# Optimization experiments

Measured on AMD Instinct MI355X. Metric: run time of the kernel, lower is better.

Reference implementation:

```python
import math
import jax, jax.numpy as jnp
import numpy as np

H = 4            # num_attention_heads
EPS = 1e-5       # InstanceNorm / LayerNorm eps (torch default)


def _inorm(x):
    # nn.InstanceNorm1d applied to (N, S, d): normalizes over the last dim per (item, token), no affine
    m = jnp.mean(x, axis=-1, keepdims=True)
    v = jnp.var(x, axis=-1, keepdims=True)
    return (x - m) / jnp.sqrt(v + EPS)


def _tree_layer(x, Wqkv, bqkv, Wo, bo, W1, b1, W2, b2):
    # x: (N, S, d) with S=2
    N, S, d = x.shape
    dh = d // H
    qkv = x @ Wqkv.T + bqkv                      # (N, S, 3d)
    q, k, v = jnp.split(qkv, 3, axis=-1)
    q = q.reshape(N, S, H, dh)
    k = k.reshape(N, S, H, dh)
    v = v.reshape(N, S, H, dh)
    scores = jnp.einsum('nqhd,nkhd->nhqk', q, k) / math.sqrt(dh)
    att = jax.nn.softmax(scores, axis=-1)
    o = jnp.einsum('nhqk,nkhd->nqhd', att, v).reshape(N, S, d)
    o = o @ Wo.T + bo
    x = _inorm(x + o)
    f = jax.nn.gelu(x @ W1.T + b1, approximate=False) @ W2.T + b2
    return _inorm(x + f)


def _mlp(x, Wa, ba, Wb, bb):
    return jax.nn.gelu(x @ Wa.T + ba, approximate=False) @ Wb.T + bb


def setup_inputs() -> dict:
    key = jax.random.key(0)
    ks = jax.random.split(key, 16)
    B, G, d, ff, L, c = 64, 1024, 256, 1024, 4, 128
    s = 0.02
    r = lambda i, shape: (jax.random.normal(ks[i], shape, jnp.float32) * s)
    return dict(
        children=jax.random.normal(ks[0], (B, G, 2, d), jnp.float32),
        roles=r(1, (3, d)),
        Wqkv=r(2, (L, 3 * d, d)), bqkv=jnp.zeros((L, 3 * d), jnp.float32),
        Wo=r(3, (L, d, d)), bo=jnp.zeros((L, d), jnp.float32),
        W1=r(4, (L, ff, d)), b1=jnp.zeros((L, ff), jnp.float32),
        W2=r(5, (L, d, ff)), b2=jnp.zeros((L, d), jnp.float32),
        Wl1=r(6, (d, d)), bl1=jnp.zeros(d, jnp.float32),
        Wl2=r(7, (c, d)), bl2=jnp.zeros(c, jnp.float32),
        Wr1=r(8, (d, d)), br1=jnp.zeros(d, jnp.float32),
        Wr2=r(9, (c, d)), br2=jnp.zeros(c, jnp.float32),
        ln_g=jnp.ones(d, jnp.float32), ln_b=jnp.zeros(d, jnp.float32),
    )


def reference(children, roles, Wqkv, bqkv, Wo, bo, W1, b1, W2, b2,
              Wl1, bl1, Wl2, bl2, Wr1, br1, Wr2, br2, ln_g, ln_b):
    B, G, _, d = children.shape
    c = Wl2.shape[0]
    L = Wqkv.shape[0]
    # flatten (batch, group) and add inside role embeddings (rows 0,1)
    x = children.reshape(B * G, 2, d) + roles[:2][None, :, :]
    for i in range(L):
        x = _tree_layer(x, Wqkv[i], bqkv[i], Wo[i], bo[i], W1[i], b1[i], W2[i], b2[i])
    out = x.reshape(B, G, 2, d)
    left_const = _mlp(out[:, :, 0, :], Wl1, bl1, Wl2, bl2)   # (B, G, c)
    right_const = _mlp(out[:, :, 1, :], Wr1, br1, Wr2, br2)  # (B, G, c)
    mat_scores = jnp.sum(left_const * right_const, axis=-1) / math.sqrt(c)
    # LayerNorm over last dim of summed children
    s = out.sum(axis=2)
    m = jnp.mean(s, axis=-1, keepdims=True)
    v = jnp.var(s, axis=-1, keepdims=True)
    src = (s - m) / jnp.sqrt(v + EPS) * ln_g + ln_b
    return mat_scores, src
```

## Files before the change

kernel.cpp:

```cpp
#include <hip/hip_runtime.h>
#include <math.h>

#define NLAYER 4
#define DMODEL 256
#define ITEMS  32
#define MROWS  64
#define XS     264
#define BS     520
#define EPSV   1e-5f
#define NWAVES 16

typedef __attribute__((ext_vector_type(8))) short short8;
typedef __attribute__((ext_vector_type(4))) float f32x4;

#define OFF_WQKV 0
#define OFF_WO   786432
#define OFF_W1   1048576
#define OFF_W2   2097152
#define OFF_WL1  3145728
#define OFF_WL2  3211264
#define OFF_WR1  3244032
#define OFF_WR2  3309568
#define WS_ELEMS 3342336

static __device__ __forceinline__ float b2f(short s) {
  return __uint_as_float(((unsigned)(unsigned short)s) << 16);
}
static __device__ __forceinline__ short f2bf(float f) {
  unsigned u = __float_as_uint(f);
  return (short)((u + 0x7fffu + ((u >> 16) & 1u)) >> 16);
}
static __device__ __forceinline__ float gelu_f(float x) {
  return 0.5f * x * (1.0f + erff(x * 0.70710678118654752f));
}

template<int MT, int PAIR>
static __device__ void gemm_lds(const short* A, int as, int rmul, int radd,
                                const short* __restrict__ W,
                                const float* __restrict__ bias,
                                short* Out, int oc0, int oro,
                                int N, int act, int tid)
{
  const int wave = tid >> 6;
  const int lane = tid & 63;
  const int lm = lane & 15;
  const int q  = lane >> 4;
  const int ntiles = N >> 4;
  const f32x4 z = {0.f, 0.f, 0.f, 0.f};
  for (int nb = wave * PAIR; nb < ntiles; nb += NWAVES * PAIR) {
    f32x4 acc[MT][PAIR];
    #pragma unroll
    for (int mt = 0; mt < MT; ++mt)
      #pragma unroll
      for (int p = 0; p < PAIR; ++p) acc[mt][p] = z;
    #pragma unroll 4
    for (int kt = 0; kt < 256; kt += 32) {
      short8 b[PAIR];
      #pragma unroll
      for (int p = 0; p < PAIR; ++p)
        b[p] = *(const short8*)(W + ((nb + p) * 16 + lm) * 256 + kt + q * 8);
      #pragma unroll
      for (int mt = 0; mt < MT; ++mt) {
        short8 a = *(const short8*)(A + (rmul * (mt * 16 + lm) + radd) * as + kt + q * 8);
        #pragma unroll
        for (int p = 0; p < PAIR; ++p)
          acc[mt][p] = __builtin_amdgcn_mfma_f32_16x16x32_bf16(a, b[p], acc[mt][p], 0, 0, 0);
      }
    }
    #pragma unroll
    for (int mt = 0; mt < MT; ++mt) {
      #pragma unroll
      for (int p = 0; p < PAIR; ++p) {
        int col = (nb + p) * 16 + lm;
        float bv = bias[col];
        #pragma unroll
        for (int r = 0; r < 4; ++r) {
          float v = acc[mt][p][r] + bv;
          if (act) v = gelu_f(v);
          Out[(oro + mt * 16 + q * 4 + r) * BS + oc0 + col] = f2bf(v);
        }
      }
    }
  }
}

static __device__ void gemm_acc512(f32x4 acc[4], const short* A,
                                   const short* __restrict__ W, int wc0, int tid)
{
  const int wave = tid >> 6, lane = tid & 63;
  const int lm = lane & 15, q = lane >> 4;
  #pragma unroll 2
  for (int kt = 0; kt < 512; kt += 32) {
    short8 b = *(const short8*)(W + (wave * 16 + lm) * 1024 + wc0 + kt + q * 8);
    #pragma unroll
    for (int mt = 0; mt < 4; ++mt) {
      short8 a = *(const short8*)(A + (mt * 16 + lm) * BS + kt + q * 8);
      acc[mt] = __builtin_amdgcn_mfma_f32_16x16x32_bf16(a, b, acc[mt], 0, 0, 0);
    }
  }
}

static __device__ void inorm_pass(short* Xs_, const short* Bf_, bool addx, int tid)
{
  if (tid >= MROWS * 4) return;
  int r = tid >> 2, sub = tid & 3;
  const short* bp = Bf_ + r * BS + sub * 64;
  short* xp = Xs_ + r * XS + sub * 64;
  float sum = 0.f, sq = 0.f;
  for (int e = 0; e < 64; ++e) {
    float v = b2f(bp[e]);
    if (addx) v += b2f(xp[e]);
    sum += v; sq += v * v;
  }
  sum += __shfl_xor(sum, 1); sq += __shfl_xor(sq, 1);
  sum += __shfl_xor(sum, 2); sq += __shfl_xor(sq, 2);
  float mean = sum * (1.f / 256.f);
  float rstd = rsqrtf(sq * (1.f / 256.f) - mean * mean + EPSV);
  for (int e = 0; e < 64; ++e) {
    float v = b2f(bp[e]);
    if (addx) v += b2f(xp[e]);
    xp[e] = f2bf((v - mean) * rstd);
  }
}

struct PrepArgs {
  const float* src[8];
  int n[8];
  int off[8];
};

__global__ void prep_weights(PrepArgs pa, short* __restrict__ dst, int total)
{
  int idx = blockIdx.x * 256 + threadIdx.x;
  if (idx >= total) return;
  int j = 0, off = idx;
  while (j < 7 && off >= pa.n[j]) { off -= pa.n[j]; ++j; }
  dst[pa.off[j] + off] = f2bf(pa.src[j][off]);
}

__global__ __launch_bounds__(1024)
void fused_encoder(const float* __restrict__ children,
                   const float* __restrict__ roles,
                   const short* __restrict__ ws,
                   const float* __restrict__ g_bqkv,
                   const float* __restrict__ g_bo,
                   const float* __restrict__ g_b1,
                   const float* __restrict__ g_b2,
                   const float* __restrict__ g_bl1, const float* __restrict__ g_bl2,
                   const float* __restrict__ g_br1, const float* __restrict__ g_br2,
                   const float* __restrict__ g_lng, const float* __restrict__ g_lnb,
                   float* __restrict__ out)
{
  __shared__ __align__(16) short Xs[MROWS * XS];
  __shared__ __align__(16) short Bf[MROWS * BS];
  __shared__ float Att[ITEMS * 16];

  const int tid = threadIdx.x;
  const int bid = blockIdx.x;

  {
    const float* src = children + (long)bid * MROWS * DMODEL;
    for (int e = tid * 4; e < MROWS * DMODEL; e += 4096) {
      int row = e >> 8, col = e & 255;
      float4 v = *(const float4*)(src + e);
      const float* rl = roles + (row & 1) * DMODEL + col;
      short* xp = Xs + row * XS + col;
      xp[0] = f2bf(v.x + rl[0]);
      xp[1] = f2bf(v.y + rl[1]);
      xp[2] = f2bf(v.z + rl[2]);
      xp[3] = f2bf(v.w + rl[3]);
    }
  }
  __syncthreads();

  for (int l = 0; l < NLAYER; ++l) {
    const short* Wqkv = ws + OFF_WQKV + l * 768 * 256;
    const short* Wo   = ws + OFF_WO   + l * 256 * 256;
    const short* W1   = ws + OFF_W1   + l * 1024 * 256;
    const short* W2   = ws + OFF_W2   + l * 256 * 1024;

    gemm_lds<4, 2>(Xs, XS, 1, 0, Wqkv, g_bqkv + l * 768, Bf, 0, 0, 512, 0, tid);
    __syncthreads();

    if (tid < ITEMS * 8) {
      int i = tid >> 3, h = (tid >> 1) & 3, tk = tid & 1;
      const short* qp = Bf + (2 * i + tk) * BS + h * 64;
      const short* k0 = Bf + (2 * i    ) * BS + 256 + h * 64;
      const short* k1 = Bf + (2 * i + 1) * BS + 256 + h * 64;
      float s0 = 0.f, s1 = 0.f;
      for (int e = 0; e < 64; ++e) {
        float qv = b2f(qp[e]);
        s0 += qv * b2f(k0[e]);
        s1 += qv * b2f(k1[e]);
      }
      s0 *= 0.125f; s1 *= 0.125f;
      float mx = fmaxf(s0, s1);
      float e0 = __expf(s0 - mx), e1 = __expf(s1 - mx);
      float inv = 1.f / (e0 + e1);
      float* ap = Att + ((i * 4 + h) * 2 + tk) * 2;
      ap[0] = e0 * inv; ap[1] = e1 * inv;
    }
    __syncthreads();

    gemm_lds<4, 1>(Xs, XS, 1, 0, Wqkv + 512 * 256, g_bqkv + l * 768 + 512, Bf, 0, 0, 256, 0, tid);
    __syncthreads();

    if (tid < MROWS * 4) {
      int r = tid >> 2, h = tid & 3;
      int i = r >> 1, tk = r & 1;
      const float* ap = Att + ((i * 4 + h) * 2 + tk) * 2;
      float a0 = ap[0], a1 = ap[1];
      const short* v0 = Bf + (2 * i) * BS + h * 64;
      const short* v1 = Bf + (2 * i + 1) * BS + h * 64;
      short* op = Bf + r * BS + 256 + h * 64;
      for (int e = 0; e < 64; ++e)
        op[e] = f2bf(a0 * b2f(v0[e]) + a1 * b2f(v1[e]));
    }
    __syncthreads();

    gemm_lds<4, 1>(Bf + 256, BS, 1, 0, Wo, g_bo + l * 256, Bf, 0, 0, 256, 0, tid);
    __syncthreads();
    inorm_pass(Xs, Bf, true, tid);
    __syncthreads();

    f32x4 facc[4];
    {
      const f32x4 z = {0.f, 0.f, 0.f, 0.f};
      #pragma unroll
      for (int mt = 0; mt < 4; ++mt) facc[mt] = z;
    }
    for (int ch = 0; ch < 2; ++ch) {
      gemm_lds<4, 2>(Xs, XS, 1, 0, W1 + ch * 512 * 256, g_b1 + l * 1024 + ch * 512,
                     Bf, 0, 0, 512, 1, tid);
      __syncthreads();
      gemm_acc512(facc, Bf, W2, ch * 512, tid);
      __syncthreads();
    }
    {
      const int wave = tid >> 6, lane = tid & 63, lm = lane & 15, q = lane >> 4;
      int col = wave * 16 + lm;
      float bv = g_b2[l * 256 + col];
      #pragma unroll
      for (int mt = 0; mt < 4; ++mt) {
        #pragma unroll
        for (int r = 0; r < 4; ++r) {
          int row = mt * 16 + q * 4 + r;
          Bf[row * BS + col] = f2bf(facc[mt][r] + bv + b2f(Xs[row * XS + col]));
        }
      }
    }
    __syncthreads();
    inorm_pass(Xs, Bf, false, tid);
    __syncthreads();
  }

  gemm_lds<2, 1>(Xs, XS, 2, 0, ws + OFF_WL1, g_bl1, Bf, 0, 0, 256, 1, tid);
  gemm_lds<2, 1>(Xs, XS, 2, 1, ws + OFF_WR1, g_br1, Bf, 256, 0, 256, 1, tid);
  __syncthreads();
  gemm_lds<2, 1>(Bf, BS, 1, 0, ws + OFF_WL2, g_bl2, Bf, 0, 32, 128, 0, tid);
  gemm_lds<2, 1>(Bf + 256, BS, 1, 0, ws + OFF_WR2, g_br2, Bf, 128, 32, 128, 0, tid);
  __syncthreads();

  if (tid < ITEMS * 8) {
    int i = tid >> 3, sub = tid & 7;
    const short* lp = Bf + (32 + i) * BS + sub * 16;
    float acc = 0.f;
    for (int j = 0; j < 16; ++j) acc += b2f(lp[j]) * b2f(lp[128 + j]);
    acc += __shfl_xor(acc, 1);
    acc += __shfl_xor(acc, 2);
    acc += __shfl_xor(acc, 4);
    if (sub == 0) out[bid * ITEMS + i] = acc * 0.088388347648318447f;
  }
  if (tid < ITEMS * 8) {
    int i = tid >> 3, sub = tid & 7;
    const short* x0 = Xs + (2 * i) * XS + sub * 32;
    const short* x1 = Xs + (2 * i + 1) * XS + sub * 32;
    float sum = 0.f, sq = 0.f;
    for (int e = 0; e < 32; ++e) {
      float v = b2f(x0[e]) + b2f(x1[e]);
      sum += v; sq += v * v;
    }
    sum += __shfl_xor(sum, 1); sq += __shfl_xor(sq, 1);
    sum += __shfl_xor(sum, 2); sq += __shfl_xor(sq, 2);
    sum += __shfl_xor(sum, 4); sq += __shfl_xor(sq, 4);
    float mean = sum * (1.f / 256.f);
    float rstd = rsqrtf(sq * (1.f / 256.f) - mean * mean + EPSV);
    float* op = out + 65536 + ((long)bid * ITEMS + i) * DMODEL + sub * 32;
    for (int e = 0; e < 32; ++e) {
      int c = sub * 32 + e;
      float v = b2f(x0[e]) + b2f(x1[e]);
      op[e] = (v - mean) * rstd * g_lng[c] + g_lnb[c];
    }
  }
}

extern "C" void kernel_launch(void* const* d_in, const int* in_sizes, int n_in,
                              void* d_out, int out_size, void* d_ws, size_t ws_size,
                              hipStream_t stream)
{
  (void)in_sizes; (void)n_in; (void)out_size; (void)ws_size;
  const float* children = (const float*)d_in[0];
  const float* roles    = (const float*)d_in[1];
  const float* Wqkv     = (const float*)d_in[2];
  const float* bqkv     = (const float*)d_in[3];
  const float* Wo       = (const float*)d_in[4];
  const float* bo       = (const float*)d_in[5];
  const float* W1       = (const float*)d_in[6];
  const float* b1       = (const float*)d_in[7];
  const float* W2       = (const float*)d_in[8];
  const float* b2       = (const float*)d_in[9];
  const float* Wl1      = (const float*)d_in[10];
  const float* bl1      = (const float*)d_in[11];
  const float* Wl2      = (const float*)d_in[12];
  const float* bl2      = (const float*)d_in[13];
  const float* Wr1      = (const float*)d_in[14];
  const float* br1      = (const float*)d_in[15];
  const float* Wr2      = (const float*)d_in[16];
  const float* br2      = (const float*)d_in[17];
  const float* ln_g     = (const float*)d_in[18];
  const float* ln_b     = (const float*)d_in[19];

  short* ws = (short*)d_ws;

  PrepArgs pa;
  pa.src[0] = Wqkv; pa.n[0] = 786432;  pa.off[0] = OFF_WQKV;
  pa.src[1] = Wo;   pa.n[1] = 262144;  pa.off[1] = OFF_WO;
  pa.src[2] = W1;   pa.n[2] = 1048576; pa.off[2] = OFF_W1;
  pa.src[3] = W2;   pa.n[3] = 1048576; pa.off[3] = OFF_W2;
  pa.src[4] = Wl1;  pa.n[4] = 65536;   pa.off[4] = OFF_WL1;
  pa.src[5] = Wl2;  pa.n[5] = 32768;   pa.off[5] = OFF_WL2;
  pa.src[6] = Wr1;  pa.n[6] = 65536;   pa.off[6] = OFF_WR1;
  pa.src[7] = Wr2;  pa.n[7] = 32768;   pa.off[7] = OFF_WR2;

  prep_weights<<<(WS_ELEMS + 255) / 256, 256, 0, stream>>>(pa, ws, WS_ELEMS);
  fused_encoder<<<2048, 1024, 0, stream>>>(children, roles, ws,
      bqkv, bo, b1, b2, bl1, bl2, br1, br2, ln_g, ln_b, (float*)d_out);
}
```

Baseline: 2.416 ms.

## Fuse QKV projection into one GEMM, merge attention apply, prefetch weights

Widens the LDS scratch buffer so Q, K and V are produced by a single 768-wide GEMM. This removes the separate V GEMM, one barrier and the Att scratch array, and softmax and the weighted V sum now happen in the same thread pass. The GEMM inner loops are fully unrolled with a software prefetch of the next weight fragment to hide global-load latency. The tail MLP GEMMs split waves between the left and right branches so they run concurrently. The costs are more LDS per block and more registers from unrolling, and the launch-bounds hint changes.

```diff
diff --git a/kernel.cpp b/kernel.cpp
--- a/kernel.cpp
+++ b/kernel.cpp
@@ -6,7 +6,7 @@
 #define ITEMS  32
 #define MROWS  64
 #define XS     264
-#define BS     520
+#define BS     776
 #define EPSV   1e-5f
 #define NWAVES 16
 
@@ -34,7 +34,7 @@
   return 0.5f * x * (1.0f + erff(x * 0.70710678118654752f));
 }
 
-template<int MT, int PAIR>
+template<int MT, int PAIR, int WBASE, int WN>
 static __device__ void gemm_lds(const short* A, int as, int rmul, int radd,
                                 const short* __restrict__ W,
                                 const float* __restrict__ bias,
@@ -42,29 +42,40 @@
                                 int N, int act, int tid)
 {
   const int wave = tid >> 6;
+  if (WN != NWAVES && (wave < WBASE || wave >= WBASE + WN)) return;
   const int lane = tid & 63;
   const int lm = lane & 15;
   const int q  = lane >> 4;
   const int ntiles = N >> 4;
   const f32x4 z = {0.f, 0.f, 0.f, 0.f};
-  for (int nb = wave * PAIR; nb < ntiles; nb += NWAVES * PAIR) {
+  for (int nb = (wave - WBASE) * PAIR; nb < ntiles; nb += WN * PAIR) {
     f32x4 acc[MT][PAIR];
     #pragma unroll
     for (int mt = 0; mt < MT; ++mt)
       #pragma unroll
       for (int p = 0; p < PAIR; ++p) acc[mt][p] = z;
-    #pragma unroll 4
+    short8 b[PAIR];
+    #pragma unroll
+    for (int p = 0; p < PAIR; ++p)
+      b[p] = *(const short8*)(W + ((nb + p) * 16 + lm) * 256 + q * 8);
+    #pragma unroll
     for (int kt = 0; kt < 256; kt += 32) {
-      short8 b[PAIR];
-      #pragma unroll
-      for (int p = 0; p < PAIR; ++p)
-        b[p] = *(const short8*)(W + ((nb + p) * 16 + lm) * 256 + kt + q * 8);
+      short8 bn[PAIR];
+      if (kt < 224) {
+        #pragma unroll
+        for (int p = 0; p < PAIR; ++p)
+          bn[p] = *(const short8*)(W + ((nb + p) * 16 + lm) * 256 + kt + 32 + q * 8);
+      }
       #pragma unroll
       for (int mt = 0; mt < MT; ++mt) {
         short8 a = *(const short8*)(A + (rmul * (mt * 16 + lm) + radd) * as + kt + q * 8);
         #pragma unroll
         for (int p = 0; p < PAIR; ++p)
           acc[mt][p] = __builtin_amdgcn_mfma_f32_16x16x32_bf16(a, b[p], acc[mt][p], 0, 0, 0);
+      }
+      if (kt < 224) {
+        #pragma unroll
+        for (int p = 0; p < PAIR; ++p) b[p] = bn[p];
       }
     }
     #pragma unroll
@@ -89,14 +100,18 @@
 {
   const int wave = tid >> 6, lane = tid & 63;
   const int lm = lane & 15, q = lane >> 4;
-  #pragma unroll 2
+  const short* wrow = W + (wave * 16 + lm) * 1024 + wc0 + q * 8;
+  short8 b = *(const short8*)(wrow);
+  #pragma unroll
   for (int kt = 0; kt < 512; kt += 32) {
-    short8 b = *(const short8*)(W + (wave * 16 + lm) * 1024 + wc0 + kt + q * 8);
+    short8 bn;
+    if (kt < 480) bn = *(const short8*)(wrow + kt + 32);
     #pragma unroll
     for (int mt = 0; mt < 4; ++mt) {
       short8 a = *(const short8*)(A + (mt * 16 + lm) * BS + kt + q * 8);
       acc[mt] = __builtin_amdgcn_mfma_f32_16x16x32_bf16(a, b, acc[mt], 0, 0, 0);
     }
+    if (kt < 480) b = bn;
   }
 }
 
@@ -138,7 +153,7 @@
   dst[pa.off[j] + off] = f2bf(pa.src[j][off]);
 }
 
-__global__ __launch_bounds__(1024)
+__global__ __launch_bounds__(1024, 4)
 void fused_encoder(const float* __restrict__ children,
                    const float* __restrict__ roles,
                    const short* __restrict__ ws,
@@ -153,7 +168,6 @@
 {
   __shared__ __align__(16) short Xs[MROWS * XS];
   __shared__ __align__(16) short Bf[MROWS * BS];
-  __shared__ float Att[ITEMS * 16];
 
   const int tid = threadIdx.x;
   const int bid = blockIdx.x;
@@ -179,7 +193,7 @@
     const short* W1   = ws + OFF_W1   + l * 1024 * 256;
     const short* W2   = ws + OFF_W2   + l * 256 * 1024;
 
-    gemm_lds<4, 2>(Xs, XS, 1, 0, Wqkv, g_bqkv + l * 768, Bf, 0, 0, 512, 0, tid);
+    gemm_lds<4, 3, 0, NWAVES>(Xs, XS, 1, 0, Wqkv, g_bqkv + l * 768, Bf, 0, 0, 768, 0, tid);
     __syncthreads();
 
     if (tid < ITEMS * 8) {
@@ -197,30 +211,18 @@
       float mx = fmaxf(s0, s1);
       float e0 = __expf(s0 - mx), e1 = __expf(s1 - mx);
       float inv = 1.f / (e0 + e1);
-      float* ap = Att + ((i * 4 + h) * 2 + tk) * 2;
-      ap[0] = e0 * inv; ap[1] = e1 * inv;
-    }
-    __syncthreads();
-
-    gemm_lds<4, 1>(Xs, XS, 1, 0, Wqkv + 512 * 256, g_bqkv + l * 768 + 512, Bf, 0, 0, 256, 0, tid);
-    __syncthreads();
-
-    if (tid < MROWS * 4) {
-      int r = tid >> 2, h = tid & 3;
-      int i = r >> 1, tk = r & 1;
-      const float* ap = Att + ((i * 4 + h) * 2 + tk) * 2;
-      float a0 = ap[0], a1 = ap[1];
-      const short* v0 = Bf + (2 * i) * BS + h * 64;
-      const short* v1 = Bf + (2 * i + 1) * BS + h * 64;
-      short* op = Bf + r * BS + 256 + h * 64;
+      float a0 = e0 * inv, a1 = e1 * inv;
+      const short* v0 = Bf + (2 * i    ) * BS + 512 + h * 64;
+      const short* v1 = Bf + (2 * i + 1) * BS + 512 + h * 64;
+      short* op = Bf + (2 * i + tk) * BS + h * 64;
       for (int e = 0; e < 64; ++e)
         op[e] = f2bf(a0 * b2f(v0[e]) + a1 * b2f(v1[e]));
     }
     __syncthreads();
 
-    gemm_lds<4, 1>(Bf + 256, BS, 1, 0, Wo, g_bo + l * 256, Bf, 0, 0, 256, 0, tid);
-    __syncthreads();
-    inorm_pass(Xs, Bf, true, tid);
+    gemm_lds<4, 1, 0, NWAVES>(Bf, BS, 1, 0, Wo, g_bo + l * 256, Bf, 256, 0, 256, 0, tid);
+    __syncthreads();
+    inorm_pass(Xs, Bf + 256, true, tid);
     __syncthreads();
 
     f32x4 facc[4];
@@ -230,8 +232,8 @@
       for (int mt = 0; mt < 4; ++mt) facc[mt] = z;
     }
     for (int ch = 0; ch < 2; ++ch) {
-      gemm_lds<4, 2>(Xs, XS, 1, 0, W1 + ch * 512 * 256, g_b1 + l * 1024 + ch * 512,
-                     Bf, 0, 0, 512, 1, tid);
+      gemm_lds<4, 2, 0, NWAVES>(Xs, XS, 1, 0, W1 + ch * 512 * 256, g_b1 + l * 1024 + ch * 512,
+                                Bf, 0, 0, 512, 1, tid);
       __syncthreads();
       gemm_acc512(facc, Bf, W2, ch * 512, tid);
       __syncthreads();
@@ -254,11 +256,11 @@
     __syncthreads();
   }
 
-  gemm_lds<2, 1>(Xs, XS, 2, 0, ws + OFF_WL1, g_bl1, Bf, 0, 0, 256, 1, tid);
-  gemm_lds<2, 1>(Xs, XS, 2, 1, ws + OFF_WR1, g_br1, Bf, 256, 0, 256, 1, tid);
+  gemm_lds<2, 2, 0, 8>(Xs, XS, 2, 0, ws + OFF_WL1, g_bl1, Bf, 0, 0, 256, 1, tid);
+  gemm_lds<2, 2, 8, 8>(Xs, XS, 2, 1, ws + OFF_WR1, g_br1, Bf, 256, 0, 256, 1, tid);
   __syncthreads();
-  gemm_lds<2, 1>(Bf, BS, 1, 0, ws + OFF_WL2, g_bl2, Bf, 0, 32, 128, 0, tid);
-  gemm_lds<2, 1>(Bf + 256, BS, 1, 0, ws + OFF_WR2, g_br2, Bf, 128, 32, 128, 0, tid);
+  gemm_lds<2, 1, 0, 8>(Bf, BS, 1, 0, ws + OFF_WL2, g_bl2, Bf, 0, 32, 128, 0, tid);
+  gemm_lds<2, 1, 8, 8>(Bf + 256, BS, 1, 0, ws + OFF_WR2, g_br2, Bf, 128, 32, 128, 0, tid);
   __syncthreads();
 
   if (tid < ITEMS * 8) {
```

Result: slower. 2.584 ms (+7.0%).
